# Kernel tuning notes

Hardware: AMD Instinct MI355X
Metric: run time of the kernel (lower is better)

Reference implementation:

```python
import jax, jax.numpy as jnp
import numpy as np
import math

HEADS = 16
SPH = 64      # size_per_head
KEY = 64      # key_size (defaults to size_per_head)
EMB = 1024
STEP = 3


def extract_seq_patches(x, kernel_size, step):
    # x: [B, L, D] -> [B, L, kernel_size, D]; patch j at pos t is x_pad[t - p_left + j*step]
    B, L, D = x.shape
    k_size = kernel_size + (step - 1) * (kernel_size - 1)
    p_right = (k_size - 1) // 2
    p_left = k_size - 1 - p_right
    xp = jnp.pad(x, ((0, 0), (p_left, p_right), (0, 0)))
    xs = [xp[:, i:i + L] for i in range(0, k_size, step)]  # kernel_size slices
    return jnp.stack(xs, axis=2)


def setup_inputs() -> dict:
    key = jax.random.key(0)
    kx, kq, kk, kv = jax.random.split(key, 4)
    B, L = 2, 4096
    x = jax.random.normal(kx, (B, L, EMB), dtype=jnp.float32)
    W_q = jax.random.normal(kq, (EMB, HEADS * KEY), dtype=jnp.float32) * 0.02
    W_k = jax.random.normal(kk, (EMB, HEADS * KEY), dtype=jnp.float32) * 0.02
    W_v = jax.random.normal(kv, (EMB, HEADS * SPH), dtype=jnp.float32) * 0.02
    return {"x": x, "W_q": W_q, "W_k": W_k, "W_v": W_v}


def _forward(x, W_q, W_k, W_v):
    B, L, D = x.shape
    pad_len = STEP - L % STEP
    x = jnp.pad(x, ((0, 0), (0, pad_len), (0, 0)))
    new_len = L + pad_len
    blocks = new_len // STEP
    q = x @ W_q  # [B, new_len, H*KEY]
    k = x @ W_k
    v = x @ W_v
    ksz = 1 + 2 * (STEP - 1)  # kernel_size = 5
    kp = extract_seq_patches(k, ksz, STEP)  # [B, new_len, ksz, H*KEY]
    vp = extract_seq_patches(v, ksz, STEP)
    # reshape to [B, H, step, blocks, d]
    q = q.reshape(B, blocks, STEP, HEADS, KEY).transpose(0, 3, 2, 1, 4)
    kb = k.reshape(B, blocks, STEP, HEADS, KEY).transpose(0, 3, 2, 1, 4)
    vb = v.reshape(B, blocks, STEP, HEADS, SPH).transpose(0, 3, 2, 1, 4)
    # neighbor patches: [B, H, step, blocks, ksz, d]
    kp = kp.reshape(B, blocks, STEP, ksz, HEADS, KEY).transpose(0, 4, 2, 1, 3, 5)
    vp = vp.reshape(B, blocks, STEP, ksz, HEADS, SPH).transpose(0, 4, 2, 1, 3, 5)
    scale = 1.0 / math.sqrt(KEY)
    # strided attention over blocks (same residue mod step): [B,H,step,blocks,blocks]
    a = jnp.einsum('bhsqk,bhspk->bhsqp', q, kb) * scale
    # block-local neighbor attention: [B,H,step,blocks,ksz]
    ap = jnp.einsum('bhsqk,bhsqnk->bhsqn', q, kp) * scale
    A = jax.nn.softmax(jnp.concatenate([a, ap], axis=-1), axis=-1)
    a, ap = A[..., :blocks], A[..., blocks:]
    o = (jnp.einsum('bhsqp,bhspd->bhsqd', a, vb)
         + jnp.einsum('bhsqn,bhsqnd->bhsqd', ap, vp))
    o = o.transpose(0, 3, 2, 1, 4).reshape(B, new_len, HEADS * SPH)
    return o[:, :L]


def reference(x, W_q, W_k, W_v):
    return _forward(x, W_q, W_k, W_v)
```

## Files before the change

kernel.cpp:

```cpp
#include <hip/hip_runtime.h>
#include <hip/hip_bf16.h>

typedef unsigned int u32;
typedef unsigned short u16;
typedef short s8v __attribute__((ext_vector_type(8)));
typedef short s4v __attribute__((ext_vector_type(4)));
typedef float f4v __attribute__((ext_vector_type(4)));
typedef u32 u32x2 __attribute__((ext_vector_type(2)));

#define NBLK 1366
#define VROW 1376
#define QSCALE 0.18033688011112042f

__device__ __forceinline__ u16 f2b(float f) {
  u32 u = __builtin_bit_cast(u32, f);
  u = (u + 0x7FFFu + ((u >> 16) & 1u)) >> 16;
  return (u16)u;
}

__device__ __forceinline__ u32 cvtpk(float a, float b) {
  u32 r;
  asm("v_cvt_pk_bf16_f32 %0, %1, %2" : "=v"(r) : "v"(a), "v"(b));
  return r;
}

__device__ __forceinline__ float fexp2(float x) {
#if defined(__has_builtin)
#if __has_builtin(__builtin_amdgcn_exp2f)
  return __builtin_amdgcn_exp2f(x);
#define FEXP2_DONE 1
#endif
#endif
#ifndef FEXP2_DONE
  float r;
  asm("v_exp_f32 %0, %1" : "=v"(r) : "v"(x));
  return r;
#endif
}

__device__ __forceinline__ void gll16(const void* g, void* l) {
  __builtin_amdgcn_global_load_lds(
      (const __attribute__((address_space(1))) u32*)g,
      (__attribute__((address_space(3))) u32*)l, 16, 0, 0);
}

__device__ __forceinline__ f4v mfma32(s8v a, s8v b, f4v c) {
  return __builtin_amdgcn_mfma_f32_16x16x32_bf16(a, b, c, 0, 0, 0);
}

__device__ __forceinline__ f4v mfma16(s4v a, s4v b, f4v c) {
#if defined(__has_builtin)
#if __has_builtin(__builtin_amdgcn_mfma_f32_16x16x16bf16_1k)
#define MFMA16_BUILTIN 1
#endif
#endif
#ifdef MFMA16_BUILTIN
  return __builtin_amdgcn_mfma_f32_16x16x16bf16_1k(a, b, c, 0, 0, 0);
#else
  f4v d;
  asm("v_mfma_f32_16x16x16_bf16 %0, %1, %2, %3" : "=v"(d) : "v"(a), "v"(b), "v"(c));
  return d;
#endif
}

__global__ __launch_bounds__(256) void k_convert_x(const float* __restrict__ x,
                                                   u16* __restrict__ xb) {
  int gid = blockIdx.x * 256 + threadIdx.x;
  long base = (long)gid * 8;
  if (base >= 8320L * 1024L) return;
  int m = (int)(base >> 10);
  int c = (int)(base & 1023);
  int b = m / 4098;
  int t = m - b * 4098;
  s8v pack;
  if (m < 8196 && t < 4096) {
    const float* src = x + ((size_t)b * 4096 + t) * 1024 + c;
    float4 v0 = *(const float4*)(src);
    float4 v1 = *(const float4*)(src + 4);
    pack[0] = (short)f2b(v0.x); pack[1] = (short)f2b(v0.y);
    pack[2] = (short)f2b(v0.z); pack[3] = (short)f2b(v0.w);
    pack[4] = (short)f2b(v1.x); pack[5] = (short)f2b(v1.y);
    pack[6] = (short)f2b(v1.z); pack[7] = (short)f2b(v1.w);
  } else {
#pragma unroll
    for (int i = 0; i < 8; ++i) pack[i] = 0;
  }
  *(s8v*)(xb + base) = pack;
}

__global__ __launch_bounds__(256) void k_transpose_w(const float* __restrict__ Wq,
                                                     const float* __restrict__ Wk,
                                                     const float* __restrict__ Wv,
                                                     u16* __restrict__ Wt) {
  const float* W = (blockIdx.z == 0) ? Wq : ((blockIdx.z == 1) ? Wk : Wv);
  u16* dst = Wt + (size_t)blockIdx.z * 1024 * 1024;
  __shared__ float tile[32][33];
  int n0 = blockIdx.x * 32, k0 = blockIdx.y * 32;
  int tx = threadIdx.x, ty = threadIdx.y;
#pragma unroll
  for (int i = 0; i < 4; ++i)
    tile[ty + i * 8][tx] = W[(size_t)(k0 + ty + i * 8) * 1024 + n0 + tx];
  __syncthreads();
#pragma unroll
  for (int i = 0; i < 4; ++i)
    dst[(size_t)(n0 + ty + i * 8) * 1024 + k0 + tx] = f2b(tile[tx][ty + i * 8]);
}

__global__ __launch_bounds__(256) void k_gemm_qkv(const u16* __restrict__ xb,
                                                  const u16* __restrict__ Wt,
                                                  u16* __restrict__ Qp,
                                                  u16* __restrict__ Kp,
                                                  u16* __restrict__ Vt) {
  const int zid = blockIdx.z;
  const int m0 = blockIdx.x * 128;
  const int n0 = blockIdx.y * 128;
  const u16* Bg = Wt + (size_t)zid * 1024 * 1024 + (size_t)n0 * 1024;

  __shared__ __align__(16) u16 shl[16384];
  u16* A0 = shl;
  u16* A1 = shl + 4096;
  u16* B0 = shl + 8192;
  u16* B1 = shl + 12288;

  const int tid = threadIdx.x;
  const int lane = tid & 63;
  const int w = tid >> 6;
  const int wr = w >> 1, wc = w & 1;
  const int lo = lane & 15, g = lane >> 4;

  const int lrow = lane >> 2;
  const int csrc = (lane & 3) ^ ((lane >> 3) & 3);
  const int rsw = (g ^ ((lo >> 1) & 3)) << 4;

  f4v acc[4][4];
#pragma unroll
  for (int i = 0; i < 4; ++i)
#pragma unroll
    for (int j = 0; j < 4; ++j) {
      f4v z = {0.f, 0.f, 0.f, 0.f};
      acc[i][j] = z;
    }

  auto stage = [&](int kt, u16* Ab, u16* Bb) {
#pragma unroll
    for (int c = 0; c < 2; ++c) {
      int rloc = w * 32 + c * 16 + lrow;
      gll16(xb + (size_t)(m0 + rloc) * 1024 + kt + csrc * 8,
            Ab + (w * 32 + c * 16) * 32);
      gll16(Bg + (size_t)rloc * 1024 + kt + csrc * 8,
            Bb + (w * 32 + c * 16) * 32);
    }
  };

  auto compute = [&](const u16* Ab, const u16* Bb) {
    s8v af[4], bf[4];
#pragma unroll
    for (int i = 0; i < 4; ++i) {
      int ar = wr * 64 + i * 16 + lo;
      af[i] = *(const s8v*)((const char*)Ab + ar * 64 + rsw);
      int br = wc * 64 + i * 16 + lo;
      bf[i] = *(const s8v*)((const char*)Bb + br * 64 + rsw);
    }
#pragma unroll
    for (int i = 0; i < 4; ++i)
#pragma unroll
      for (int j = 0; j < 4; ++j)
        acc[i][j] = mfma32(af[i], bf[j], acc[i][j]);
  };

  stage(0, A0, B0);
  __syncthreads();
#pragma unroll 1
  for (int kk = 0; kk < 16; ++kk) {
    int kt = kk * 2 * 32;
    stage(kt + 32, A1, B1);
    compute(A0, B0);
    __syncthreads();
    if (kk < 15) stage(kt + 64, A0, B0);
    compute(A1, B1);
    __syncthreads();
  }

  const float esc = (zid == 0) ? QSCALE : 1.0f;
  if (zid != 2) {
    u16* dq = (zid == 0) ? Qp : Kp;
#pragma unroll
    for (int i = 0; i < 4; ++i) {
#pragma unroll
      for (int r = 0; r < 4; ++r) {
        int m = m0 + wr * 64 + i * 16 + g * 4 + r;
        if (m >= 8196) continue;
        int b = m / 4098;
        int t = m - b * 4098;
        int s = t % 3;
        int p = t / 3;
        int cb = (b * 3 + s) * 16;
#pragma unroll
        for (int j = 0; j < 4; ++j) {
          int n = n0 + wc * 64 + j * 16 + lo;
          int h = n >> 6, d = n & 63;
          dq[(size_t)((cb + h) * NBLK + p) * 64 + d] = f2b(acc[i][j][r] * esc);
        }
      }
    }
  } else {
    u16* tile = shl;
#pragma unroll
    for (int i = 0; i < 4; ++i)
#pragma unroll
      for (int r = 0; r < 4; ++r) {
        int ml = wr * 64 + i * 16 + g * 4 + r;
#pragma unroll
        for (int j = 0; j < 4; ++j) {
          int nl = wc * 64 + j * 16 + lo;
          tile[ml * 128 + nl] = f2b(acc[i][j][r]);
        }
      }
    __syncthreads();
    for (int pair = tid; pair < 384; pair += 256) {
      int nl = pair & 127;
      int s = pair >> 7;
      int n = n0 + nl;
      int h = n >> 6, d = n & 63;
      for (int b = 0; b < 2; ++b) {
        int mlo = m0 > b * 4098 ? m0 : b * 4098;
        int cap = b * 4098 + 4096;
        int mhi = (m0 + 128 < cap) ? m0 + 128 : cap;
        if (mlo >= mhi) continue;
        int t_lo = mlo - b * 4098;
        int add = (s - (t_lo % 3) + 3) % 3;
        int t = t_lo + add;
        int tend = mhi - b * 4098;
        u16* dst = Vt + (size_t)(((b * 3 + s) * 16 + h) * 64 + d) * VROW;
        for (; t < tend; t += 3)
          dst[t / 3] = tile[(b * 4098 + t - m0) * 128 + nl];
      }
    }
  }
}

__global__ __launch_bounds__(256) void k_attn(const u16* __restrict__ Qp,
                                              const u16* __restrict__ Kp,
                                              const u16* __restrict__ Vt,
                                              float* __restrict__ out) {
  const int wg = blockIdx.x;
  const int idx = (wg & 7) * 264 + (wg >> 3);
  const int combo = idx / 22;
  const int q0 = (idx % 22) * 64;
  const int b = combo / 48;
  const int rem = combo - b * 48;
  const int s = rem >> 4;
  const int h = rem & 15;
  const int tid = threadIdx.x, lane = tid & 63, w = tid >> 6;
  const int lo = lane & 15, g = lane >> 4;

  const u16* Qg = Qp + (size_t)combo * (NBLK * 64);
  const u16* Kg = Kp + (size_t)combo * (NBLK * 64);
  const u16* Vg = Vt + (size_t)combo * (64 * VROW);

  __shared__ __align__(16) u16 Kl[64 * 64];
  __shared__ __align__(16) u16 Vl[64 * 64];

  const int pq_e = q0 + w * 16 + lo;
  const int qc = (pq_e < NBLK) ? pq_e : (NBLK - 1);
  s8v qf0 = *(const s8v*)(Qg + (size_t)qc * 64 + g * 8);
  s8v qf1 = *(const s8v*)(Qg + (size_t)qc * 64 + 32 + g * 8);

  s4v onesf;
  onesf[0] = onesf[1] = onesf[2] = onesf[3] = (short)0x3F80;

  f4v oacc[4];
#pragma unroll
  for (int i = 0; i < 4; ++i) {
    f4v z = {0.f, 0.f, 0.f, 0.f};
    oacc[i] = z;
  }
  f4v den_acc = {0.f, 0.f, 0.f, 0.f};

  const int lrow = lane >> 3;
  const int schunk = (lane & 7) ^ lrow;

  for (int j0 = 0; j0 < NBLK; j0 += 64) {
    __syncthreads();
#pragma unroll
    for (int c = 0; c < 2; ++c) {
      int rloc = w * 16 + c * 8 + lrow;
      gll16(Kg + (size_t)(j0 + rloc) * 64 + schunk * 8, Kl + (w * 16 + c * 8) * 64);
      gll16(Vg + (size_t)rloc * VROW + j0 + schunk * 8, Vl + (w * 16 + c * 8) * 64);
    }
    __syncthreads();

    f4v sacc[4];
    __builtin_amdgcn_s_setprio(1);
#pragma unroll
    for (int kb = 0; kb < 4; ++kb) {
      f4v z = {0.f, 0.f, 0.f, 0.f};
      int row = kb * 16 + lo;
      int sw = (row & 7) << 4;
      s8v kf0 = *(const s8v*)((const char*)Kl + row * 128 + ((g * 16) ^ sw));
      s8v kf1 = *(const s8v*)((const char*)Kl + row * 128 + ((64 + g * 16) ^ sw));
      z = mfma32(kf0, qf0, z);
      sacc[kb] = mfma32(kf1, qf1, z);
    }
    __builtin_amdgcn_s_setprio(0);

    s4v ef[4];
    const bool special = (j0 >= q0 - 64 && j0 <= q0 + 64) || (j0 + 64 > NBLK);
    if (special) {
#pragma unroll
      for (int kb = 0; kb < 4; ++kb) {
        float e[4];
#pragma unroll
        for (int r = 0; r < 4; ++r) {
          int j = j0 + kb * 16 + g * 4 + r;
          float ev = fexp2(sacc[kb][r]);
          int dd = j - pq_e;
          float fac = (j < NBLK) ? (((dd <= 2) && (dd >= -2)) ? 2.f : 1.f) : 0.f;
          e[r] = ev * fac;
        }
        u32x2 w2;
        w2[0] = cvtpk(e[0], e[1]);
        w2[1] = cvtpk(e[2], e[3]);
        ef[kb] = __builtin_bit_cast(s4v, w2);
      }
    } else {
#pragma unroll
      for (int kb = 0; kb < 4; ++kb) {
        u32x2 w2;
        w2[0] = cvtpk(fexp2(sacc[kb][0]), fexp2(sacc[kb][1]));
        w2[1] = cvtpk(fexp2(sacc[kb][2]), fexp2(sacc[kb][3]));
        ef[kb] = __builtin_bit_cast(s4v, w2);
      }
    }

    __builtin_amdgcn_s_setprio(1);
#pragma unroll
    for (int kb = 0; kb < 4; ++kb)
      den_acc = mfma16(ef[kb], onesf, den_acc);
#pragma unroll
    for (int db = 0; db < 4; ++db) {
      int row = db * 16 + lo;
      int sw = (row & 7) << 4;
#pragma unroll
      for (int kb = 0; kb < 4; ++kb) {
        s4v vf = *(const s4v*)((const char*)Vl + row * 128 + ((kb * 32 + g * 8) ^ sw));
        oacc[db] = mfma16(ef[kb], vf, oacc[db]);
      }
    }
    __builtin_amdgcn_s_setprio(0);
  }

  const int hbase = h * 64;
#pragma unroll
  for (int r = 0; r < 4; ++r) {
    int pq = q0 + w * 16 + g * 4 + r;
    float dden = den_acc[r];
    dden += (pq == 0 || pq == NBLK - 1) ? 2.f : ((pq == 1 || pq == NBLK - 2) ? 1.f : 0.f);
    float rr = 1.f / dden;
    int t = 3 * pq + s;
    if (pq < NBLK && t < 4096) {
      float* orow = out + ((size_t)b * 4096 + t) * 1024 + hbase;
#pragma unroll
      for (int db = 0; db < 4; ++db)
        orow[db * 16 + lo] = oacc[db][r] * rr;
    }
  }
}

extern "C" void kernel_launch(void* const* d_in, const int* in_sizes, int n_in,
                              void* d_out, int out_size, void* d_ws, size_t ws_size,
                              hipStream_t stream) {
  const float* x  = (const float*)d_in[0];
  const float* Wq = (const float*)d_in[1];
  const float* Wk = (const float*)d_in[2];
  const float* Wv = (const float*)d_in[3];
  float* out = (float*)d_out;

  u16* ws = (u16*)d_ws;
  u16* xb = ws;
  u16* Wt = xb + 8519680;
  u16* Qp = Wt + 3145728;
  u16* Kp = Qp + 8392704;
  u16* Vt = Kp + 8392704;

  k_convert_x<<<4160, 256, 0, stream>>>(x, xb);
  k_transpose_w<<<dim3(32, 32, 3), dim3(32, 8), 0, stream>>>(Wq, Wk, Wv, Wt);
  hipMemsetAsync(Vt, 0, (size_t)(8454144 + 256) * sizeof(u16), stream);
  k_gemm_qkv<<<dim3(65, 8, 3), 256, 0, stream>>>(xb, Wt, Qp, Kp, Vt);
  k_attn<<<dim3(2112), 256, 0, stream>>>(Qp, Kp, Vt, out);
}
```

Baseline: 222.5 us.

## Deepen async LDS prefetch pipelines in QKV GEMM and attention kernels

The QKV GEMM moves from a 2-stage to a 3-stage LDS ring, so two tiles are in flight while one is computed. It also replaces __syncthreads with partial vmcnt waits plus raw barriers and raises wave priority around the MFMA loop. The attention kernel goes from load-sync-compute to double-buffered K/V tiles, so the next tile's global-to-LDS copy overlaps the current compute. The cost is more LDS per block, which may lower occupancy, plus hand-counted vmcnt values that must match the number of outstanding loads.

```diff
diff --git a/kernel.cpp b/kernel.cpp
--- a/kernel.cpp
+++ b/kernel.cpp
@@ -116,11 +116,7 @@
   const int n0 = blockIdx.y * 128;
   const u16* Bg = Wt + (size_t)zid * 1024 * 1024 + (size_t)n0 * 1024;
 
-  __shared__ __align__(16) u16 shl[16384];
-  u16* A0 = shl;
-  u16* A1 = shl + 4096;
-  u16* B0 = shl + 8192;
-  u16* B1 = shl + 12288;
+  __shared__ __align__(16) u16 shl[24576];
 
   const int tid = threadIdx.x;
   const int lane = tid & 63;
@@ -141,7 +137,10 @@
       acc[i][j] = z;
     }
 
-  auto stage = [&](int kt, u16* Ab, u16* Bb) {
+  auto stage = [&](int tile) {
+    u16* Ab = shl + (tile % 3) * 8192;
+    u16* Bb = Ab + 4096;
+    int kt = tile * 32;
 #pragma unroll
     for (int c = 0; c < 2; ++c) {
       int rloc = w * 32 + c * 16 + lrow;
@@ -152,7 +151,9 @@
     }
   };
 
-  auto compute = [&](const u16* Ab, const u16* Bb) {
+  auto compute = [&](int tile) {
+    const u16* Ab = shl + (tile % 3) * 8192;
+    const u16* Bb = Ab + 4096;
     s8v af[4], bf[4];
 #pragma unroll
     for (int i = 0; i < 4; ++i) {
@@ -161,25 +162,42 @@
       int br = wc * 64 + i * 16 + lo;
       bf[i] = *(const s8v*)((const char*)Bb + br * 64 + rsw);
     }
+    __builtin_amdgcn_s_setprio(1);
 #pragma unroll
     for (int i = 0; i < 4; ++i)
 #pragma unroll
       for (int j = 0; j < 4; ++j)
         acc[i][j] = mfma32(af[i], bf[j], acc[i][j]);
+    __builtin_amdgcn_s_setprio(0);
   };
 
-  stage(0, A0, B0);
+#define WBAR(VM)                                            \
+  asm volatile("s_waitcnt vmcnt(" VM ")" ::: "memory");     \
+  __builtin_amdgcn_s_barrier();                             \
+  asm volatile("" ::: "memory");
+#define TBAR                                                \
+  asm volatile("s_waitcnt lgkmcnt(0)" ::: "memory");        \
+  __builtin_amdgcn_s_barrier();                             \
+  asm volatile("" ::: "memory");
+
+  stage(0);
+  stage(1);
+#pragma unroll 1
+  for (int t = 0; t < 30; ++t) {
+    stage(t + 2);
+    WBAR("8")
+    compute(t);
+    TBAR
+  }
+  WBAR("4")
+  compute(30);
+  TBAR
+  WBAR("0")
+  compute(31);
   __syncthreads();
-#pragma unroll 1
-  for (int kk = 0; kk < 16; ++kk) {
-    int kt = kk * 2 * 32;
-    stage(kt + 32, A1, B1);
-    compute(A0, B0);
-    __syncthreads();
-    if (kk < 15) stage(kt + 64, A0, B0);
-    compute(A1, B1);
-    __syncthreads();
-  }
+
+#undef WBAR
+#undef TBAR
 
   const float esc = (zid == 0) ? QSCALE : 1.0f;
   if (zid != 2) {
@@ -258,8 +276,7 @@
   const u16* Kg = Kp + (size_t)combo * (NBLK * 64);
   const u16* Vg = Vt + (size_t)combo * (64 * VROW);
 
-  __shared__ __align__(16) u16 Kl[64 * 64];
-  __shared__ __align__(16) u16 Vl[64 * 64];
+  __shared__ __align__(16) u16 att[16384];
 
   const int pq_e = q0 + w * 16 + lo;
   const int qc = (pq_e < NBLK) ? pq_e : (NBLK - 1);
@@ -280,15 +297,22 @@
   const int lrow = lane >> 3;
   const int schunk = (lane & 7) ^ lrow;
 
-  for (int j0 = 0; j0 < NBLK; j0 += 64) {
-    __syncthreads();
+  auto stage = [&](int jt) {
+    int j0 = jt * 64;
+    u16* Kl = att + (jt & 1) * 8192;
+    u16* Vl = Kl + 4096;
 #pragma unroll
     for (int c = 0; c < 2; ++c) {
       int rloc = w * 16 + c * 8 + lrow;
       gll16(Kg + (size_t)(j0 + rloc) * 64 + schunk * 8, Kl + (w * 16 + c * 8) * 64);
       gll16(Vg + (size_t)rloc * VROW + j0 + schunk * 8, Vl + (w * 16 + c * 8) * 64);
     }
-    __syncthreads();
+  };
+
+  auto compute = [&](int jt) {
+    const int j0 = jt * 64;
+    const u16* Kl = att + (jt & 1) * 8192;
+    const u16* Vl = Kl + 4096;
 
     f4v sacc[4];
     __builtin_amdgcn_s_setprio(1);
@@ -348,7 +372,30 @@
       }
     }
     __builtin_amdgcn_s_setprio(0);
-  }
+  };
+
+#define WBAR(VM)                                            \
+  asm volatile("s_waitcnt vmcnt(" VM ")" ::: "memory");     \
+  __builtin_amdgcn_s_barrier();                             \
+  asm volatile("" ::: "memory");
+#define TBAR                                                \
+  asm volatile("s_waitcnt lgkmcnt(0)" ::: "memory");        \
+  __builtin_amdgcn_s_barrier();                             \
+  asm volatile("" ::: "memory");
+
+  stage(0);
+#pragma unroll 1
+  for (int jt = 0; jt < 21; ++jt) {
+    stage(jt + 1);
+    WBAR("2")
+    compute(jt);
+    TBAR
+  }
+  WBAR("0")
+  compute(21);
+
+#undef WBAR
+#undef TBAR
 
   const int hbase = h * 64;
 #pragma unroll
```

Result: no change. 224.7 us (+1.0%).
